# Kernel optimization log

Hardware: AMD Instinct MI355X
Metric: run time of the kernel (lower is better)

Reference implementation:

```python
import jax, jax.numpy as jnp
import numpy as np

NUM_TYPES = 8
NUM_REL = 6
N_LAYERS = 2


def setup_inputs() -> dict:
    key = jax.random.key(0)
    ks = jax.random.split(key, 8)
    N, E, D_in, D = 20000, 320000, 512, 256
    node_feature = jax.random.normal(ks[0], (N, D_in), dtype=jnp.float32)
    node_type = jax.random.randint(ks[1], (N,), 0, NUM_TYPES)
    edge_index = jax.random.randint(ks[2], (2, E), 0, N)
    edge_type = jax.random.randint(ks[3], (E,), 0, NUM_REL)
    node_position = jnp.arange(N)
    # learned params
    adapt_W = jax.random.normal(ks[4], (NUM_TYPES, D, D_in), dtype=jnp.float32) * 0.02
    adapt_b = jnp.zeros((NUM_TYPES, D), dtype=jnp.float32)
    W_rel = jax.random.normal(ks[5], (N_LAYERS, NUM_REL, D, D), dtype=jnp.float32) * 0.05
    W_self = jax.random.normal(ks[6], (N_LAYERS, D, D), dtype=jnp.float32) * 0.05
    b_self = jnp.zeros((N_LAYERS, D), dtype=jnp.float32)
    return {
        "node_feature": node_feature,
        "node_type": node_type,
        "edge_index": edge_index,
        "edge_type": edge_type,
        "node_position": node_position,
        "adapt_W": adapt_W,
        "adapt_b": adapt_b,
        "W_rel": W_rel,
        "W_self": W_self,
        "b_self": b_self,
    }


def reference(node_feature, node_type, edge_index, edge_type, node_position,
              adapt_W, adapt_b, W_rel, W_self, b_self):
    N = node_feature.shape[0]
    D = adapt_W.shape[1]
    # per-node-type adaptation: res[i] = tanh(W_{t_i} x_i + b_{t_i})
    # (original loops over types with boolean gather/scatter; here we mask-select)
    h = jnp.zeros((N, D), dtype=node_feature.dtype)
    for t in range(NUM_TYPES):
        y = jnp.tanh(node_feature @ adapt_W[t].T + adapt_b[t])
        h = jnp.where((node_type == t)[:, None], y, h)
    # dropout p=0.0 -> identity
    src, dst = edge_index[0], edge_index[1]
    deg = jax.ops.segment_sum(jnp.ones(src.shape, h.dtype), dst, num_segments=N)
    inv_deg = (1.0 / jnp.maximum(deg, 1.0))[:, None]  # [N,1]
    # relational GNN layer stack (stand-in for unseen GraphConv)
    for l in range(N_LAYERS):
        hr = jnp.einsum('nd,rde->rne', h, W_rel[l])      # [R,N,D]
        msg = hr[edge_type, src]                          # [E,D] gather by (relation, src)
        agg = jax.ops.segment_sum(msg, dst, num_segments=N)
        h = jax.nn.relu(agg * inv_deg + h @ W_self[l] + b_self[l])
    return h
```

## Files before the change

### kernel.cpp

```cpp
#include <hip/hip_runtime.h>

constexpr int NTYPES = 8;
constexpr int NREL   = 6;
constexpr int NSLOT  = 7;
constexpr int D      = 256;
constexpr int DIN    = 512;
constexpr int LDH    = NSLOT * D;

using short8 = __attribute__((ext_vector_type(8))) short;
using f32x4  = __attribute__((ext_vector_type(4))) float;

__device__ __forceinline__ ushort f2b(float f) {
  unsigned u = __float_as_uint(f);
  u += 0x7fffu + ((u >> 16) & 1u);
  return (ushort)(u >> 16);
}
__device__ __forceinline__ float b2f(unsigned bits16) {
  return __uint_as_float(bits16 << 16);
}

#define GLOAD_LDS16(g, l)                                              \
  __builtin_amdgcn_global_load_lds(                                    \
      (__attribute__((address_space(1))) void*)(g),                    \
      (__attribute__((address_space(3))) void*)(l), 16, 0, 0)

__global__ void k_zero(int* __restrict__ p, int n) {
  int i = blockIdx.x * blockDim.x + threadIdx.x;
  if (i < n) p[i] = 0;
}

__global__ void k_prep_mega(const float* __restrict__ X, ushort* __restrict__ Xb,
                            const float* __restrict__ Wa, ushort* __restrict__ Wab,
                            const float* __restrict__ Wrel, const float* __restrict__ Wself,
                            ushort* __restrict__ Wcat,
                            const int* __restrict__ ntype, int* __restrict__ blockcnt,
                            const int* __restrict__ dst, int* __restrict__ deg,
                            int N, int E, int nx, int nw, int np, int nbN,
                            int n4x, int n4w) {
  __shared__ int cnt[NTYPES];
  const int b = blockIdx.x;
  const int tid = threadIdx.x;
  if (b < nx) {
    int i = b * 256 + tid;
    if (i < n4x) {
      float4 v = ((const float4*)X)[i];
      ushort4 o; o.x = f2b(v.x); o.y = f2b(v.y); o.z = f2b(v.z); o.w = f2b(v.w);
      ((ushort4*)Xb)[i] = o;
    }
  } else if (b < nx + nw) {
    int i = (b - nx) * 256 + tid;
    if (i < n4w) {
      float4 v = ((const float4*)Wa)[i];
      ushort4 o; o.x = f2b(v.x); o.y = f2b(v.y); o.z = f2b(v.z); o.w = f2b(v.w);
      ((ushort4*)Wab)[i] = o;
    }
  } else if (b < nx + nw + np) {
    int local = b - nx - nw;
    int l = local / (NSLOT * 256);
    int s = (local % (NSLOT * 256)) / 256;
    int o = (local % 256) * 256 + tid;
    int e = o >> 8, d = o & 255;
    float v = (s < NREL) ? Wrel[(((size_t)l * NREL + s) * D + d) * D + e]
                         : Wself[((size_t)l * D + d) * D + e];
    Wcat[(((size_t)l * NSLOT + s) * D + e) * D + d] = f2b(v);
  } else if (b < nx + nw + np + nbN) {
    const int bb = b - nx - nw - np;
    int i = bb * 256 + tid;
    if (tid < NTYPES) cnt[tid] = 0;
    __syncthreads();
    int t = (i < N) ? ntype[i] : -1;
#pragma unroll
    for (int ty = 0; ty < NTYPES; ++ty) {
      unsigned long long m = __ballot(t == ty);
      if ((tid & 63) == 0 && m) atomicAdd(&cnt[ty], __popcll(m));
    }
    __syncthreads();
    if (tid < NTYPES) blockcnt[bb * NTYPES + tid] = cnt[tid];
  } else {
    int e = (b - nx - nw - np - nbN) * 256 + tid;
    if (e < E) atomicAdd(&deg[dst[e]], 1);
  }
}

__global__ __launch_bounds__(512)
void k_scan2(const int* __restrict__ blockcnt, int* __restrict__ boffset,
             int* __restrict__ cnt, int* __restrict__ offt, int nbN,
             const int* __restrict__ deg, int* __restrict__ rowptr,
             int* __restrict__ bsum, int N) {
  if (blockIdx.x == 0) {
    __shared__ int tot[NTYPES];
    __shared__ int base[NTYPES];
    const int w = threadIdx.x >> 6;
    const int l = threadIdx.x & 63;
    int v0 = (l < nbN) ? blockcnt[l * NTYPES + w] : 0;
    int v1 = (64 + l < nbN) ? blockcnt[(64 + l) * NTYPES + w] : 0;
    int s0 = v0;
#pragma unroll
    for (int o = 1; o < 64; o <<= 1) { int t = __shfl_up(s0, o); if (l >= o) s0 += t; }
    int total0 = __shfl(s0, 63);
    int s1 = v1;
#pragma unroll
    for (int o = 1; o < 64; o <<= 1) { int t = __shfl_up(s1, o); if (l >= o) s1 += t; }
    s1 += total0;
    int totalw = __shfl(s1, 63);
    if (l == 0) { tot[w] = totalw; cnt[w] = totalw; }
    __syncthreads();
    if (threadIdx.x == 0) {
      int s = 0;
      for (int ty = 0; ty < NTYPES; ++ty) { base[ty] = s; offt[ty] = s; s += tot[ty]; }
    }
    __syncthreads();
    const int bs = base[w];
    if (l < nbN) boffset[l * NTYPES + w] = bs + s0 - v0;
    if (64 + l < nbN) boffset[(64 + l) * NTYPES + w] = bs + s1 - v1;
  } else {
    __shared__ int sm[512];
    const int bb = blockIdx.x - 1;
    const int t = threadIdx.x;
    int i = bb * 512 + t;
    int v = (i < N) ? deg[i] : 0;
    sm[t] = v;
    __syncthreads();
    for (int o = 1; o < 512; o <<= 1) {
      int x = (t >= o) ? sm[t - o] : 0;
      __syncthreads();
      sm[t] += x;
      __syncthreads();
    }
    if (i < N) rowptr[i] = sm[t] - v;
    if (t == 511) bsum[bb] = sm[511];
  }
}

__global__ void k_scatter_bsum(const int* __restrict__ ntype, const int* __restrict__ boffset,
                               int* __restrict__ perm, int N, int nbN,
                               int* __restrict__ bsum, int nbs) {
  __shared__ int cur[NTYPES];
  const int b = blockIdx.x;
  if (b < nbN) {
    int i = b * 256 + threadIdx.x;
    if (threadIdx.x < NTYPES) cur[threadIdx.x] = boffset[b * NTYPES + threadIdx.x];
    __syncthreads();
    int t = (i < N) ? ntype[i] : -1;
    int lane = threadIdx.x & 63;
#pragma unroll
    for (int ty = 0; ty < NTYPES; ++ty) {
      unsigned long long m = __ballot(t == ty);
      if (m) {
        int wbase = 0;
        if (lane == 0) wbase = atomicAdd(&cur[ty], __popcll(m));
        wbase = __shfl(wbase, 0);
        if (t == ty) {
          int rank = __popcll(m & ((1ull << lane) - 1ull));
          perm[wbase + rank] = i;
        }
      }
    }
  } else if (threadIdx.x < 64) {
    const int l = threadIdx.x;
    int v0 = (l < nbs) ? bsum[l] : 0;
    int s0 = v0;
#pragma unroll
    for (int o = 1; o < 64; o <<= 1) { int t = __shfl_up(s0, o); if (l >= o) s0 += t; }
    if (l < nbs) bsum[l] = s0 - v0;
  }
}

__global__ void k_scan_add(int* __restrict__ rowptr, int* __restrict__ cursor,
                           const int* __restrict__ bsum, const int* __restrict__ deg,
                           float* __restrict__ inv, int N, int E) {
  int i = blockIdx.x * 256 + threadIdx.x;
  if (i < N) {
    int r = rowptr[i] + bsum[i >> 9];
    rowptr[i] = r;
    cursor[i] = r;
    inv[i] = 1.0f / fmaxf((float)deg[i], 1.0f);
  }
  if (i == 0) rowptr[N] = E;
}

template <int BM, int BN, int NTN, int KDIM, bool ADAPT, bool SORT, int OCC>
__global__ __launch_bounds__(256, OCC)
void k_mfma_gemm(const ushort* __restrict__ A, const ushort* __restrict__ B,
                 const float* __restrict__ bias,
                 const int* __restrict__ perm, const int* __restrict__ cnt,
                 const int* __restrict__ off,
                 ushort* __restrict__ Cout, int N, int ldC, int nwg,
                 const int* __restrict__ s_src, const int* __restrict__ s_dst,
                 const int* __restrict__ s_et, int* __restrict__ s_cursor,
                 int* __restrict__ s_epack, int s_E) {
  if (SORT && (int)blockIdx.x >= nwg) {
    int e = ((int)blockIdx.x - nwg) * 256 + threadIdx.x;
    if (e < s_E) {
      int pos = atomicAdd(&s_cursor[s_dst[e]], 1);
      s_epack[pos] = (s_src[e] << 3) | s_et[e];
    }
    return;
  }

  const int qq = nwg >> 3, rr = nwg & 7;
  const int xcd = blockIdx.x & 7, idx = blockIdx.x >> 3;
  const int wgid = (xcd < rr ? xcd * (qq + 1) : rr * (qq + 1) + (xcd - rr) * qq) + idx;

  int mcnt = N, mtile, ntile;
  const int* permt = nullptr;
  const ushort* Bt = B;
  const float* biast = bias;
  if (ADAPT) {
    const int mt = nwg / (NTYPES * NTN);
    const int t = wgid / (mt * NTN);
    const int rem = wgid % (mt * NTN);
    mtile = rem / NTN;
    ntile = rem % NTN;
    mcnt = cnt[t];
    permt = perm + off[t];
    Bt = B + (size_t)t * D * KDIM;
    biast = bias + t * D;
  } else {
    mtile = wgid / NTN;
    ntile = wgid % NTN;
  }
  const int m0 = mtile * BM;
  if (m0 >= mcnt) return;
  const int n0 = ntile * BN;

  __shared__ ushort SM[3][2][BM * 32];
  static_assert(BM * BN <= 3 * 2 * BM * 32, "C tile must fit in staging LDS");

  const int tid  = threadIdx.x;
  const int lane = tid & 63;
  const int w    = tid >> 6;
  constexpr int FR = BM / 32;
  constexpr int FC = BN / 32;
  const int wr   = (w >> 1) * (BM / 2);
  const int wc   = (w & 1) * (BN / 2);

  constexpr int PW = BM / 16 / 4;
  const ushort* gA[PW];
  const ushort* gB[PW];
  int lo[PW];
#pragma unroll
  for (int u = 0; u < PW; ++u) {
    const int c  = w + u * 4;
    const int r  = c * 16 + (lane >> 2);
    const int sl = (lane & 3) ^ ((r >> 1) & 3);
    int ga;
    if (ADAPT) ga = permt[min(m0 + r, mcnt - 1)];
    else       ga = min(m0 + r, N - 1);
    gA[u] = A + (size_t)ga * KDIM + sl * 8;
    gB[u] = Bt + (size_t)(n0 + r) * KDIM + sl * 8;
    lo[u] = c * 512;
  }

  auto STAGE = [&](int k0, int buf) {
#pragma unroll
    for (int u = 0; u < PW; ++u) {
      GLOAD_LDS16(gA[u] + k0, &SM[buf][0][lo[u]]);
      GLOAD_LDS16(gB[u] + k0, &SM[buf][1][lo[u]]);
    }
  };
  auto WAIT_LPS = [&]() {
    if constexpr (PW == 1) asm volatile("s_waitcnt vmcnt(2)" ::: "memory");
    else                   asm volatile("s_waitcnt vmcnt(4)" ::: "memory");
  };

  f32x4 acc[FR][FC] = {};
  const int r15 = lane & 15;
  const int g   = lane >> 4;
  const int gsw = g ^ ((r15 >> 1) & 3);

  auto COMPUTE = [&](int buf) {
    short8 af[FR], bf[FC];
#pragma unroll
    for (int i = 0; i < FR; ++i)
      af[i] = *(const short8*)(&SM[buf][0][(wr + i * 16 + r15) * 32 + gsw * 8]);
#pragma unroll
    for (int j = 0; j < FC; ++j)
      bf[j] = *(const short8*)(&SM[buf][1][(wc + j * 16 + r15) * 32 + gsw * 8]);
#pragma unroll
    for (int i = 0; i < FR; ++i)
#pragma unroll
      for (int j = 0; j < FC; ++j)
        acc[i][j] = __builtin_amdgcn_mfma_f32_16x16x32_bf16(af[i], bf[j], acc[i][j], 0, 0, 0);
  };

  constexpr int NT = KDIM / 32;
  static_assert(NT >= 3, "pipeline needs NT >= 3");

  STAGE(0, 0);
  STAGE(32, 1);

#pragma unroll
  for (int kt = 0; kt < NT - 1; ++kt) {
    WAIT_LPS();
    __builtin_amdgcn_s_barrier();
    __builtin_amdgcn_sched_barrier(0);
    COMPUTE(kt % 3);
    if (kt + 2 < NT) STAGE((kt + 2) * 32, (kt + 2) % 3);
  }
  asm volatile("s_waitcnt vmcnt(0)" ::: "memory");
  __builtin_amdgcn_s_barrier();
  __builtin_amdgcn_sched_barrier(0);
  COMPUTE((NT - 1) % 3);

  __syncthreads();
  ushort* Ct = (ushort*)SM;
#pragma unroll
  for (int i = 0; i < FR; ++i) {
#pragma unroll
    for (int q4 = 0; q4 < 4; ++q4) {
      const int row = wr + i * 16 + (lane >> 4) * 4 + q4;
#pragma unroll
      for (int j = 0; j < FC; ++j) {
        const int col = wc + j * 16 + r15;
        float v = acc[i][j][q4];
        if (ADAPT) v = tanhf(v + biast[n0 + col]);
        Ct[row * BN + col] = f2b(v);
      }
    }
  }
  __syncthreads();
  constexpr int C8 = BN / 8;
  constexpr int UNITS = BM * C8;
#pragma unroll
  for (int u0 = 0; u0 < UNITS; u0 += 256) {
    const int u = u0 + tid;
    const int row = u / C8, c8 = u % C8;
    const int rl = m0 + row;
    if (rl < mcnt) {
      const int grow = ADAPT ? permt[rl] : rl;
      *(short8*)(Cout + (size_t)grow * ldC + n0 + c8 * 8) =
          *(const short8*)(Ct + row * BN + c8 * 8);
    }
  }
}

template <bool LAST>
__global__ void k_combine(const ushort* __restrict__ Hall, const int* __restrict__ rowptr,
                          const int* __restrict__ epack, const float* __restrict__ invd,
                          const float* __restrict__ bias, void* __restrict__ outp, int N) {
  int v = blockIdx.x * 4 + (threadIdx.x >> 6);
  if (v >= N) return;
  int lane = threadIdx.x & 63;
  int e0 = rowptr[v], e1 = rowptr[v + 1];
  const uint2 s = *(const uint2*)(Hall + (size_t)v * LDH + NREL * D + lane * 4);
  float iv = invd[v];
  const float4 b4 = *(const float4*)(bias + lane * 4);

  float a0 = 0.f, a1 = 0.f, a2 = 0.f, a3 = 0.f;
  int e = e0;
  for (; e + 8 <= e1; e += 8) {
    uint2 u[8];
#pragma unroll
    for (int k = 0; k < 8; ++k) {
      int p = epack[e + k];
      u[k] = *(const uint2*)(Hall + (size_t)(p >> 3) * LDH + (p & 7) * D + lane * 4);
    }
#pragma unroll
    for (int k = 0; k < 8; ++k) {
      a0 += b2f(u[k].x & 0xffffu);
      a1 += __uint_as_float(u[k].x & 0xffff0000u);
      a2 += b2f(u[k].y & 0xffffu);
      a3 += __uint_as_float(u[k].y & 0xffff0000u);
    }
  }
  if (e + 4 <= e1) {
    uint2 u[4];
#pragma unroll
    for (int k = 0; k < 4; ++k) {
      int p = epack[e + k];
      u[k] = *(const uint2*)(Hall + (size_t)(p >> 3) * LDH + (p & 7) * D + lane * 4);
    }
#pragma unroll
    for (int k = 0; k < 4; ++k) {
      a0 += b2f(u[k].x & 0xffffu);
      a1 += __uint_as_float(u[k].x & 0xffff0000u);
      a2 += b2f(u[k].y & 0xffffu);
      a3 += __uint_as_float(u[k].y & 0xffff0000u);
    }
    e += 4;
  }
  for (; e < e1; ++e) {
    int p = epack[e];
    const uint2 u = *(const uint2*)(Hall + (size_t)(p >> 3) * LDH + (p & 7) * D + lane * 4);
    a0 += b2f(u.x & 0xffffu);
    a1 += __uint_as_float(u.x & 0xffff0000u);
    a2 += b2f(u.y & 0xffffu);
    a3 += __uint_as_float(u.y & 0xffff0000u);
  }
  float o0 = fmaxf(fmaf(a0, iv, b2f(s.x & 0xffffu)) + b4.x, 0.f);
  float o1 = fmaxf(fmaf(a1, iv, __uint_as_float(s.x & 0xffff0000u)) + b4.y, 0.f);
  float o2 = fmaxf(fmaf(a2, iv, b2f(s.y & 0xffffu)) + b4.z, 0.f);
  float o3 = fmaxf(fmaf(a3, iv, __uint_as_float(s.y & 0xffff0000u)) + b4.w, 0.f);
  if (LAST) {
    float4 o; o.x = o0; o.y = o1; o.z = o2; o.w = o3;
    ((float4*)outp)[(size_t)v * 64 + lane] = o;
  } else {
    ushort4 o; o.x = f2b(o0); o.y = f2b(o1); o.z = f2b(o2); o.w = f2b(o3);
    ((ushort4*)outp)[(size_t)v * 64 + lane] = o;
  }
}

extern "C" void kernel_launch(void* const* d_in, const int* in_sizes, int n_in,
                              void* d_out, int out_size, void* d_ws, size_t ws_size,
                              hipStream_t stream) {
  const float* X       = (const float*)d_in[0];
  const int*   ntype   = (const int*)d_in[1];
  const int*   eidx    = (const int*)d_in[2];
  const int*   etype   = (const int*)d_in[3];
  const float* adapt_W = (const float*)d_in[5];
  const float* adapt_b = (const float*)d_in[6];
  const float* W_rel   = (const float*)d_in[7];
  const float* W_self  = (const float*)d_in[8];
  const float* b_self  = (const float*)d_in[9];

  const int N = in_sizes[1];
  const int E = in_sizes[3];
  const int* src = eidx;
  const int* dst = eidx + E;

  char* ws = (char*)d_ws;
  size_t o = 0;
  auto alloc = [&](size_t bytes) { void* p = ws + o; o += (bytes + 255) & ~255ull; return p; };

  ushort* Hall  = (ushort*)alloc((size_t)N * LDH * 2);
  ushort* Xb    = Hall;
  ushort* h     = (ushort*)alloc((size_t)N * D * 2);
  ushort* Wab   = (ushort*)alloc((size_t)NTYPES * D * DIN * 2);
  ushort* Wcat  = (ushort*)alloc((size_t)2 * NSLOT * D * D * 2);
  int*   deg    = (int*)alloc((size_t)N * 4);
  float* inv    = (float*)alloc((size_t)N * 4);
  int*   perm   = (int*)alloc((size_t)N * 4);
  int*   rowptr = (int*)alloc((size_t)(N + 1) * 4);
  int*   cursor = (int*)alloc((size_t)N * 4);
  int*   epack  = (int*)alloc((size_t)E * 4);
  int*   bsum   = (int*)alloc(1024 * 4);
  int*   blockcnt = (int*)alloc((size_t)1024 * NTYPES * 4);
  int*   boffset  = (int*)alloc((size_t)1024 * NTYPES * 4);
  int*   cnt    = (int*)alloc(NTYPES * 4);
  int*   offt   = (int*)alloc(NTYPES * 4);

  const int thr = 256;
  const int nbN = (N + thr - 1) / thr;
  const int nbE = (E + thr - 1) / thr;
  const int nbN512 = (N + 511) / 512;

  k_zero<<<nbN, thr, 0, stream>>>(deg, N);

  const int n4x = N * DIN / 4;
  const int n4w = NTYPES * D * DIN / 4;
  const int nx = (n4x + thr - 1) / thr;
  const int nw = (n4w + thr - 1) / thr;
  const int np = 2 * NSLOT * (D * D / 256);
  k_prep_mega<<<nx + nw + np + nbN + nbE, thr, 0, stream>>>(
      X, Xb, adapt_W, Wab, W_rel, W_self, Wcat, ntype, blockcnt, dst, deg,
      N, E, nx, nw, np, nbN, n4x, n4w);

  k_scan2<<<1 + nbN512, 512, 0, stream>>>(blockcnt, boffset, cnt, offt, nbN,
                                          deg, rowptr, bsum, N);

  k_scatter_bsum<<<nbN + 1, thr, 0, stream>>>(ntype, boffset, perm, N, nbN, bsum, nbN512);

  k_scan_add<<<nbN, thr, 0, stream>>>(rowptr, cursor, bsum, deg, inv, N, E);

  const int mtA = (N + 63) / 64;
  const int nwgA = NTYPES * mtA * (D / 64);
  k_mfma_gemm<64, 64, D / 64, DIN, true, true, 6><<<nwgA + nbE, 256, 0, stream>>>(
      Xb, Wab, adapt_b, perm, cnt, offt, h, N, D, nwgA,
      src, dst, etype, cursor, epack, E);

  const int mtL = (N + 127) / 128;
  const int nwgL = mtL * (LDH / 128);
  for (int l = 0; l < 2; ++l) {
    const ushort* Wl = Wcat + (size_t)l * NSLOT * D * D;
    k_mfma_gemm<128, 128, LDH / 128, D, false, false, 4><<<nwgL, 256, 0, stream>>>(
        h, Wl, nullptr, nullptr, nullptr, nullptr, Hall, N, LDH, nwgL,
        nullptr, nullptr, nullptr, nullptr, nullptr, 0);
    if (l == 0)
      k_combine<false><<<(N + 3) / 4, 256, 0, stream>>>(Hall, rowptr, epack, inv,
                                                        b_self + (size_t)l * D, h, N);
    else
      k_combine<true><<<(N + 3) / 4, 256, 0, stream>>>(Hall, rowptr, epack, inv,
                                                       b_self + (size_t)l * D, d_out, N);
  }
}
```

Baseline: 187.5 us.

## Use 256x128 tiles for layer GEMM with double-buffered LDS pipeline

```diff
diff --git a/kernel.cpp b/kernel.cpp
--- a/kernel.cpp
+++ b/kernel.cpp
@@ -224,8 +224,9 @@
   if (m0 >= mcnt) return;
   const int n0 = ntile * BN;
 
-  __shared__ ushort SM[3][2][BM * 32];
-  static_assert(BM * BN <= 3 * 2 * BM * 32, "C tile must fit in staging LDS");
+  __shared__ ushort SMA[2][BM * 32];
+  __shared__ ushort SMB[2][BN * 32];
+  constexpr bool CSTAGE = (BM * BN <= 2 * BM * 32);
 
   const int tid  = threadIdx.x;
   const int lane = tid & 63;
@@ -235,12 +236,13 @@
   const int wr   = (w >> 1) * (BM / 2);
   const int wc   = (w & 1) * (BN / 2);
 
-  constexpr int PW = BM / 16 / 4;
-  const ushort* gA[PW];
-  const ushort* gB[PW];
-  int lo[PW];
-#pragma unroll
-  for (int u = 0; u < PW; ++u) {
+  constexpr int PWA = BM / 64;
+  constexpr int PWB = BN / 64;
+  const ushort* gA[PWA];
+  const ushort* gB[PWB];
+  int loA[PWA], loB[PWB];
+#pragma unroll
+  for (int u = 0; u < PWA; ++u) {
     const int c  = w + u * 4;
     const int r  = c * 16 + (lane >> 2);
     const int sl = (lane & 3) ^ ((r >> 1) & 3);
@@ -248,20 +250,22 @@
     if (ADAPT) ga = permt[min(m0 + r, mcnt - 1)];
     else       ga = min(m0 + r, N - 1);
     gA[u] = A + (size_t)ga * KDIM + sl * 8;
+    loA[u] = c * 512;
+  }
+#pragma unroll
+  for (int u = 0; u < PWB; ++u) {
+    const int c  = w + u * 4;
+    const int r  = c * 16 + (lane >> 2);
+    const int sl = (lane & 3) ^ ((r >> 1) & 3);
     gB[u] = Bt + (size_t)(n0 + r) * KDIM + sl * 8;
-    lo[u] = c * 512;
+    loB[u] = c * 512;
   }
 
   auto STAGE = [&](int k0, int buf) {
 #pragma unroll
-    for (int u = 0; u < PW; ++u) {
-      GLOAD_LDS16(gA[u] + k0, &SM[buf][0][lo[u]]);
-      GLOAD_LDS16(gB[u] + k0, &SM[buf][1][lo[u]]);
-    }
-  };
-  auto WAIT_LPS = [&]() {
-    if constexpr (PW == 1) asm volatile("s_waitcnt vmcnt(2)" ::: "memory");
-    else                   asm volatile("s_waitcnt vmcnt(4)" ::: "memory");
+    for (int u = 0; u < PWA; ++u) GLOAD_LDS16(gA[u] + k0, &SMA[buf][loA[u]]);
+#pragma unroll
+    for (int u = 0; u < PWB; ++u) GLOAD_LDS16(gB[u] + k0, &SMB[buf][loB[u]]);
   };
 
   f32x4 acc[FR][FC] = {};
@@ -269,68 +273,76 @@
   const int g   = lane >> 4;
   const int gsw = g ^ ((r15 >> 1) & 3);
 
-  auto COMPUTE = [&](int buf) {
+  STAGE(0, 0);
+  __syncthreads();
+
+  constexpr int NT = KDIM / 32;
+  int curb = 0;
+#pragma unroll
+  for (int kt = 0; kt < NT; ++kt) {
+    if (kt + 1 < NT) STAGE((kt + 1) * 32, curb ^ 1);
+
     short8 af[FR], bf[FC];
 #pragma unroll
     for (int i = 0; i < FR; ++i)
-      af[i] = *(const short8*)(&SM[buf][0][(wr + i * 16 + r15) * 32 + gsw * 8]);
+      af[i] = *(const short8*)(&SMA[curb][(wr + i * 16 + r15) * 32 + gsw * 8]);
 #pragma unroll
     for (int j = 0; j < FC; ++j)
-      bf[j] = *(const short8*)(&SM[buf][1][(wc + j * 16 + r15) * 32 + gsw * 8]);
+      bf[j] = *(const short8*)(&SMB[curb][(wc + j * 16 + r15) * 32 + gsw * 8]);
 #pragma unroll
     for (int i = 0; i < FR; ++i)
 #pragma unroll
       for (int j = 0; j < FC; ++j)
         acc[i][j] = __builtin_amdgcn_mfma_f32_16x16x32_bf16(af[i], bf[j], acc[i][j], 0, 0, 0);
-  };
-
-  constexpr int NT = KDIM / 32;
-  static_assert(NT >= 3, "pipeline needs NT >= 3");
-
-  STAGE(0, 0);
-  STAGE(32, 1);
-
-#pragma unroll
-  for (int kt = 0; kt < NT - 1; ++kt) {
-    WAIT_LPS();
-    __builtin_amdgcn_s_barrier();
-    __builtin_amdgcn_sched_barrier(0);
-    COMPUTE(kt % 3);
-    if (kt + 2 < NT) STAGE((kt + 2) * 32, (kt + 2) % 3);
-  }
-  asm volatile("s_waitcnt vmcnt(0)" ::: "memory");
-  __builtin_amdgcn_s_barrier();
-  __builtin_amdgcn_sched_barrier(0);
-  COMPUTE((NT - 1) % 3);
-
-  __syncthreads();
-  ushort* Ct = (ushort*)SM;
-#pragma unroll
-  for (int i = 0; i < FR; ++i) {
-#pragma unroll
-    for (int q4 = 0; q4 < 4; ++q4) {
-      const int row = wr + i * 16 + (lane >> 4) * 4 + q4;
-#pragma unroll
-      for (int j = 0; j < FC; ++j) {
-        const int col = wc + j * 16 + r15;
-        float v = acc[i][j][q4];
-        if (ADAPT) v = tanhf(v + biast[n0 + col]);
-        Ct[row * BN + col] = f2b(v);
+
+    __syncthreads();
+    curb ^= 1;
+  }
+
+  if constexpr (CSTAGE) {
+    ushort* Ct = (ushort*)SMA;
+#pragma unroll
+    for (int i = 0; i < FR; ++i) {
+#pragma unroll
+      for (int q4 = 0; q4 < 4; ++q4) {
+        const int row = wr + i * 16 + (lane >> 4) * 4 + q4;
+#pragma unroll
+        for (int j = 0; j < FC; ++j) {
+          const int col = wc + j * 16 + r15;
+          float v = acc[i][j][q4];
+          if (ADAPT) v = tanhf(v + biast[n0 + col]);
+          Ct[row * BN + col] = f2b(v);
+        }
       }
     }
-  }
-  __syncthreads();
-  constexpr int C8 = BN / 8;
-  constexpr int UNITS = BM * C8;
-#pragma unroll
-  for (int u0 = 0; u0 < UNITS; u0 += 256) {
-    const int u = u0 + tid;
-    const int row = u / C8, c8 = u % C8;
-    const int rl = m0 + row;
-    if (rl < mcnt) {
-      const int grow = ADAPT ? permt[rl] : rl;
-      *(short8*)(Cout + (size_t)grow * ldC + n0 + c8 * 8) =
-          *(const short8*)(Ct + row * BN + c8 * 8);
+    __syncthreads();
+    constexpr int C8 = BN / 8;
+    constexpr int UNITS = BM * C8;
+#pragma unroll
+    for (int u0 = 0; u0 < UNITS; u0 += 256) {
+      const int u = u0 + tid;
+      const int row = u / C8, c8 = u % C8;
+      const int rl = m0 + row;
+      if (rl < mcnt) {
+        const int grow = ADAPT ? permt[rl] : rl;
+        *(short8*)(Cout + (size_t)grow * ldC + n0 + c8 * 8) =
+            *(const short8*)(Ct + row * BN + c8 * 8);
+      }
+    }
+  } else {
+#pragma unroll
+    for (int i = 0; i < FR; ++i) {
+#pragma unroll
+      for (int q4 = 0; q4 < 4; ++q4) {
+        const int m = m0 + wr + i * 16 + (lane >> 4) * 4 + q4;
+        if (m < N) {
+#pragma unroll
+          for (int j = 0; j < FC; ++j) {
+            const int n = n0 + wc + j * 16 + r15;
+            Cout[(size_t)m * ldC + n] = f2b(acc[i][j][q4]);
+          }
+        }
+      }
     }
   }
 }
@@ -469,11 +481,11 @@
       Xb, Wab, adapt_b, perm, cnt, offt, h, N, D, nwgA,
       src, dst, etype, cursor, epack, E);
 
-  const int mtL = (N + 127) / 128;
+  const int mtL = (N + 255) / 256;
   const int nwgL = mtL * (LDH / 128);
   for (int l = 0; l < 2; ++l) {
     const ushort* Wl = Wcat + (size_t)l * NSLOT * D * D;
-    k_mfma_gemm<128, 128, LDH / 128, D, false, false, 4><<<nwgL, 256, 0, stream>>>(
+    k_mfma_gemm<256, 128, LDH / 128, D, false, false, 2><<<nwgL, 256, 0, stream>>>(
         h, Wl, nullptr, nullptr, nullptr, nullptr, Hall, N, LDH, nwgL,
         nullptr, nullptr, nullptr, nullptr, nullptr, 0);
     if (l == 0)
```

Measured after the change: 205.2 us. 9.4% more time.
